# Performance work log

Measured on AMD Instinct MI355X. Metric: run time of the kernel, lower is better.

Reference implementation:

```python
import jax, jax.numpy as jnp
import numpy as np

B, S, HID = 2, 2048, 2048
NH, DN, DR, DV, RANK = 16, 128, 64, 128, 512
DQK = DN + DR
SCALE = DQK ** -0.5
EPS = 1e-5


def _rope(x, theta):
    # x: [..., d] with d even; theta broadcastable to [..., d//2] (angle per pair)
    x1, x2 = x[..., 0::2], x[..., 1::2]
    c, s = jnp.cos(theta), jnp.sin(theta)
    return jnp.stack([x1 * c - x2 * s, x1 * s + x2 * c], axis=-1).reshape(x.shape)


def _layernorm(x, gamma, beta):
    mu = jnp.mean(x, axis=-1, keepdims=True)
    var = jnp.var(x, axis=-1, keepdims=True)
    return (x - mu) * jax.lax.rsqrt(var + EPS) * gamma + beta


def setup_inputs() -> dict:
    key = jax.random.key(0)
    ks = jax.random.split(key, 8)
    def xavier(k, fan_in, fan_out, gain=1.0):
        lim = gain * np.sqrt(6.0 / (fan_in + fan_out))
        return jax.random.uniform(k, (fan_in, fan_out), jnp.float32, -lim, lim)
    return {
        "hidden_states": jax.random.normal(ks[0], (B, S, HID), jnp.float32),
        "freqs_cis": jax.random.uniform(ks[1], (S, DR // 2), jnp.float32) * 2.0 * np.pi,
        "Wq": xavier(ks[2], HID, NH * DQK),                      # q_proj (stored [in,out])
        "Wkv_a": xavier(ks[3], HID, RANK + DR),                  # kv_proj_a
        "kv_gamma": jnp.ones((RANK,), jnp.float32),              # kv_norm
        "kv_beta": jnp.zeros((RANK,), jnp.float32),
        "Wkv_b": xavier(ks[4], RANK, NH * (DN + DV)),            # kv_proj_b
        "Wout": xavier(ks[5], NH * DV, HID, gain=1.0 / np.sqrt(2.0)),  # out_proj
    }


def reference(hidden_states, freqs_cis, Wq, Wkv_a, kv_gamma, kv_beta, Wkv_b, Wout):
    b, s, _ = hidden_states.shape
    max_len = freqs_cis.shape[0]
    pos = jnp.arange(s) % max_len                      # [s], position_ids=None path
    theta = freqs_cis[pos]                             # [s, DR//2]

    # Q projection, split nope/rope, partial RoPE
    q = (hidden_states @ Wq).reshape(b, s, NH, DQK)
    q_nope, q_rope = q[..., :DN], q[..., DN:]
    q_rope = _rope(q_rope, theta[None, :, None, :])    # [b,s,nh,DR]

    # Low-rank KV: compressed latent + shared rope key
    kv = hidden_states @ Wkv_a                         # [b,s,RANK+DR]
    kv_c, k_rope = kv[..., :RANK], kv[..., RANK:]
    k_rope = _rope(k_rope, theta[None, :, :])          # [b,s,DR]
    kv_c = _layernorm(kv_c, kv_gamma, kv_beta)
    kvb = (kv_c @ Wkv_b).reshape(b, s, NH, DN + DV)
    k_nope, v = kvb[..., :DN], kvb[..., DN:]
    k = jnp.concatenate(
        [k_nope, jnp.broadcast_to(k_rope[:, :, None, :], (b, s, NH, DR))], axis=-1)

    q = jnp.concatenate([q_nope, q_rope], axis=-1)     # [b,s,nh,DQK]
    scores = jnp.einsum('bthd,bshd->btsh', q, k) * SCALE
    weights = jax.nn.softmax(scores.astype(jnp.float32), axis=2).astype(q.dtype)
    attn = jnp.einsum('btsh,bshd->bthd', weights, v).reshape(b, s, NH * DV)
    return attn @ Wout
```

## Files before the change

kernel.cpp:

```cpp
#include <hip/hip_runtime.h>

#define BATCH 2
#define SEQ   2048
#define HID   2048
#define NH    16
#define DN    128
#define DR    64
#define DV    128
#define RANK  512
#define DQK   192
#define NQ    (NH*DQK)
#define NQKV  3712
#define NKVB  (NH*(DN+DV))
#define NTOK  (BATCH*SEQ)
#define SCALE_F 0.07216878364870323f

typedef __bf16 bf16x8 __attribute__((ext_vector_type(8)));
typedef float  f32x4  __attribute__((ext_vector_type(4)));
typedef unsigned int u32x4 __attribute__((ext_vector_type(4)));
typedef unsigned short u16;
typedef unsigned short u16x4 __attribute__((ext_vector_type(4)));

__device__ __forceinline__ float b2f(u16 h) {
    unsigned int u = ((unsigned int)h) << 16;
    float f; __builtin_memcpy(&f, &u, 4); return f;
}
__device__ __forceinline__ u16 f2b(float f) {
    unsigned int x; __builtin_memcpy(&x, &f, 4);
    unsigned int r = x + 0x7fffu + ((x >> 16) & 1u);
    return (u16)(r >> 16);
}
__device__ __forceinline__ bf16x8 lds_frag(const u16* p) {
    u32x4 v = *(const u32x4*)p;
    return __builtin_bit_cast(bf16x8, v);
}
__device__ __forceinline__ bf16x8 to_frag(u32x4 v) {
    return __builtin_bit_cast(bf16x8, v);
}
__device__ __forceinline__ f32x4 mfma16(bf16x8 a, bf16x8 b, f32x4 c) {
    return __builtin_amdgcn_mfma_f32_16x16x32_bf16(a, b, c, 0, 0, 0);
}
__device__ __forceinline__ void store_out(u16* p, float v) { *p = f2b(v); }
__device__ __forceinline__ void store_out(float* p, float v) { *p = v; }
__device__ __forceinline__ void gld_lds16(const u16* g, u16* l) {
    __builtin_amdgcn_global_load_lds(
        (const __attribute__((address_space(1))) unsigned int*)g,
        (__attribute__((address_space(3))) unsigned int*)l, 16, 0, 0);
}

__global__ __launch_bounds__(256) void prep_kernel(
        const float* __restrict__ hs_f, u16* __restrict__ hs,
        const float* __restrict__ Wq, const float* __restrict__ Wkva,
        const float* __restrict__ Wkvb, const float* __restrict__ Wout,
        u16* __restrict__ WqkvT, u16* __restrict__ WkvbT, u16* __restrict__ WoutT) {
    int tid = threadIdx.x;
    int bid = blockIdx.x;
    if (bid < 8192) {
        int i = bid * 256 + tid;
        f32x4 v = *(const f32x4*)(hs_f + (size_t)i * 4);
        u16 o[4];
        for (int k = 0; k < 4; k++) o[k] = f2b(v[k]);
        *(unsigned long long*)(hs + (size_t)i * 4) = *(unsigned long long*)o;
        return;
    }
    bid -= 8192;
    const float* in; u16* out; int R, C, tilesC;
    if (bid < 1536)      { in = Wq;   out = WqkvT;                       R = HID;  C = NQ;   tilesC = 48; }
    else if (bid < 1856) { bid -= 1536; in = Wkva; out = WqkvT + (size_t)NQ * HID; R = HID; C = 576; tilesC = 10; }
    else if (bid < 2368) { bid -= 1856; in = Wkvb; out = WkvbT;          R = RANK; C = NKVB; tilesC = 64; }
    else                 { bid -= 2368; in = Wout; out = WoutT;          R = HID;  C = HID;  tilesC = 32; }
    __shared__ unsigned int t32[64 * 65];
    int r0 = (bid / tilesC) * 64, c0 = (bid % tilesC) * 64;
    bool valid = (c0 < C);
    for (int i = 0; i < 4; i++) {
        int u = tid + i * 256;
        int rl = u >> 4, c4 = u & 15;
        f32x4 v = {0.f, 0.f, 0.f, 0.f};
        if (valid) v = *(const f32x4*)&in[(size_t)(r0 + rl) * C + c0 + c4 * 4];
        for (int j = 0; j < 4; j++)
            t32[(c4 * 4 + j) * 65 + rl] = f2b(v[j]);
    }
    __syncthreads();
    for (int i = 0; i < 2; i++) {
        int u = tid + i * 256;
        int cl = u >> 3, r8 = (u & 7) * 8;
        unsigned int w[8];
        for (int j = 0; j < 8; j++) w[j] = t32[cl * 65 + r8 + j];
        u32x4 pk;
        for (int j = 0; j < 4; j++) pk[j] = (w[2 * j] & 0xffffu) | (w[2 * j + 1] << 16);
        *(u32x4*)&out[(size_t)(c0 + cl) * R + r0 + r8] = pk;
    }
}

template <typename OutT>
__global__ __launch_bounds__(256) void gemm_bt(const u16* __restrict__ A,
                                               const u16* __restrict__ Bt,
                                               OutT* __restrict__ C,
                                               int K, int lda, int ldb, int ldc) {
    __shared__ u16 As[128 * 32];
    __shared__ u16 Bs[128 * 32];
    int tid = threadIdx.x, lane = tid & 63, w = tid >> 6;
    int wm = (w >> 1) * 64, wn = (w & 1) * 64;
    int g = lane >> 4, ln = lane & 15;
    int m0 = blockIdx.y * 128, n0 = blockIdx.x * 128;
    f32x4 acc[4][4] = {};
    for (int k0 = 0; k0 < K; k0 += 32) {
        for (int i = 0; i < 2; i++) {
            int ch = tid + i * 256;
            int row = ch >> 2, o = ch & 3;
            gld_lds16(&A[(size_t)(m0 + row) * lda + k0 + o * 8], &As[row * 32 + o * 8]);
            gld_lds16(&Bt[(size_t)(n0 + row) * ldb + k0 + o * 8], &Bs[row * 32 + o * 8]);
        }
        __syncthreads();
        bf16x8 af[4], bf[4];
        for (int i = 0; i < 4; i++) af[i] = lds_frag(&As[(wm + i * 16 + ln) * 32 + g * 8]);
        for (int j = 0; j < 4; j++) bf[j] = lds_frag(&Bs[(wn + j * 16 + ln) * 32 + g * 8]);
        for (int i = 0; i < 4; i++)
            for (int j = 0; j < 4; j++)
                acc[i][j] = mfma16(af[i], bf[j], acc[i][j]);
        __syncthreads();
    }
    for (int i = 0; i < 4; i++)
        for (int j = 0; j < 4; j++)
            for (int r = 0; r < 4; r++) {
                int m = m0 + wm + i * 16 + g * 4 + r;
                int n = n0 + wn + j * 16 + ln;
                store_out(&C[(size_t)m * ldc + n], acc[i][j][r]);
            }
}

__global__ void rope_q(u16* __restrict__ qkv, const float* __restrict__ freqs) {
    int token = blockIdx.x;
    int s = token & (SEQ - 1);
    int tid = threadIdx.x;
    for (int i = 0; i < 2; i++) {
        int idx = tid + i * 256;
        int hh = idx >> 5, p = idx & 31;
        float th = freqs[s * 32 + p];
        float c = __cosf(th), sn = __sinf(th);
        size_t off = (size_t)token * NQKV + hh * DQK + DN + 2 * p;
        float x1 = b2f(qkv[off]), x2 = b2f(qkv[off + 1]);
        qkv[off]     = f2b(x1 * c - x2 * sn);
        qkv[off + 1] = f2b(x1 * sn + x2 * c);
    }
}

__global__ void ln_kv(const u16* __restrict__ qkv, const float* __restrict__ gamma,
                      const float* __restrict__ beta, u16* __restrict__ kv_c) {
    int row = blockIdx.x, tid = threadIdx.x;
    size_t base = (size_t)row * NQKV + NQ;
    float x0 = b2f(qkv[base + tid]), x1 = b2f(qkv[base + 256 + tid]);
    float s = x0 + x1, q2 = x0 * x0 + x1 * x1;
    for (int o = 32; o > 0; o >>= 1) { s += __shfl_xor(s, o); q2 += __shfl_xor(q2, o); }
    __shared__ float sh[8];
    int lane = tid & 63, w = tid >> 6;
    if (lane == 0) { sh[w] = s; sh[4 + w] = q2; }
    __syncthreads();
    float S = sh[0] + sh[1] + sh[2] + sh[3];
    float Q2 = sh[4] + sh[5] + sh[6] + sh[7];
    float mu = S * (1.f / 512.f);
    float var = Q2 * (1.f / 512.f) - mu * mu;
    float rs = rsqrtf(var + 1e-5f);
    kv_c[(size_t)row * RANK + tid] =
        f2b((x0 - mu) * rs * gamma[tid] + beta[tid]);
    kv_c[(size_t)row * RANK + 256 + tid] =
        f2b((x1 - mu) * rs * gamma[256 + tid] + beta[256 + tid]);
}

__global__ void k_assemble(const u16* __restrict__ kvb, const u16* __restrict__ qkv,
                           const float* __restrict__ freqs, u16* __restrict__ Kf) {
    int token = blockIdx.x;
    int s = token & (SEQ - 1);
    int tid = threadIdx.x;
    __shared__ u16 roped[64];
    if (tid < 32) {
        int p = tid;
        float th = freqs[s * 32 + p];
        float c = __cosf(th), sn = __sinf(th);
        float x1 = b2f(qkv[(size_t)token * NQKV + NQ + RANK + 2 * p]);
        float x2 = b2f(qkv[(size_t)token * NQKV + NQ + RANK + 2 * p + 1]);
        roped[2 * p]     = f2b(x1 * c - x2 * sn);
        roped[2 * p + 1] = f2b(x1 * sn + x2 * c);
    }
    __syncthreads();
    {
        int hh = tid >> 4, d8 = (tid & 15) * 8;
        *(u32x4*)&Kf[(size_t)token * NQ + hh * DQK + d8] =
            *(const u32x4*)&kvb[(size_t)token * NKVB + hh * 256 + d8];
    }
    if (tid < 128) {
        int hh = tid >> 3, d8 = (tid & 7) * 8;
        *(u32x4*)&Kf[(size_t)token * NQ + hh * DQK + DN + d8] = *(u32x4*)&roped[d8];
    }
}

__global__ void v_transpose(const u16* __restrict__ kvb, u16* __restrict__ Vt) {
    __shared__ unsigned int t32[64 * 65];
    int st = blockIdx.x * 64, dt = blockIdx.y * 64;
    int b = blockIdx.z >> 4, h = blockIdx.z & 15;
    int tid = threadIdx.x;
    for (int i = 0; i < 2; i++) {
        int u = tid + i * 256;
        int sl = u >> 3, c8 = (u & 7) * 8;
        u32x4 v = *(const u32x4*)&kvb[((size_t)(b * SEQ + st + sl) * NH + h) * 256 + DN + dt + c8];
        for (int j = 0; j < 4; j++) {
            t32[(c8 + 2 * j) * 65 + sl]     = v[j] & 0xffffu;
            t32[(c8 + 2 * j + 1) * 65 + sl] = v[j] >> 16;
        }
    }
    __syncthreads();
    for (int i = 0; i < 2; i++) {
        int u = tid + i * 256;
        int dl = u >> 3, s8 = (u & 7) * 8;
        unsigned int w[8];
        for (int j = 0; j < 8; j++) w[j] = t32[dl * 65 + s8 + j];
        u32x4 pk;
        for (int j = 0; j < 4; j++) pk[j] = (w[2 * j] & 0xffffu) | (w[2 * j + 1] << 16);
        *(u32x4*)&Vt[((size_t)(b * NH + h) * DV + dt + dl) * SEQ + st + s8] = pk;
    }
}

#define KC    64
#define QTILE 64
#define QSTR 200
#define PSTR 72
#define VSTR 72
#define NIT  (SEQ / KC)
__global__ __launch_bounds__(256, 3) void attn_kernel(const u16* __restrict__ Q,
                                                      const u16* __restrict__ Kf,
                                                      const u16* __restrict__ Vt,
                                                      u16* __restrict__ O) {
    __shared__ u16 Ks[KC * QSTR];
    __shared__ u16 Ps[QTILE * PSTR];
    __shared__ u16 Vs[DV * VSTR];
    __shared__ float lsumLDS[2][QTILE];
    int tid = threadIdx.x, lane = tid & 63, w = tid >> 6;
    int w1 = w & 1;
    int w2 = w >> 1;
    int g = lane >> 4, ln = lane & 15;
    int qt = blockIdx.x, h = blockIdx.y, b = blockIdx.z;

    size_t qbase  = ((size_t)(b * SEQ + qt * QTILE)) * NQKV + h * DQK;
    size_t kbase0 = ((size_t)(b * SEQ) * NH + h) * DQK;
    size_t vbase  = (size_t)(b * NH + h) * DV * SEQ;

    bf16x8 bfq[2][6];
    for (int ni = 0; ni < 2; ni++)
        for (int kk = 0; kk < 6; kk++)
            bfq[ni][kk] = to_frag(*(const u32x4*)&Q[qbase +
                (size_t)(w1 * 32 + ni * 16 + ln) * NQKV + kk * 32 + g * 8]);

    u32x4 kpre[6], vpre[4];
    {
        int krow = tid >> 2;
        for (int i = 0; i < 6; i++) {
            int o = (tid & 3) + 4 * i;
            kpre[i] = *(const u32x4*)&Kf[kbase0 + (size_t)krow * NQ + o * 8];
        }
        int vrow = tid >> 1;
        for (int i = 0; i < 4; i++) {
            int o = (tid & 1) + 2 * i;
            vpre[i] = *(const u32x4*)&Vt[vbase + (size_t)vrow * SEQ + o * 8];
        }
    }
    f32x4 oacc[2][4] = {};
    float lpriv[2] = {0.f, 0.f};

    for (int kt = 0; kt < NIT; kt++) {
        {
            int krow = tid >> 2;
            for (int i = 0; i < 6; i++) {
                int o = (tid & 3) + 4 * i;
                *(u32x4*)&Ks[krow * QSTR + o * 8] = kpre[i];
            }
            int vrow = tid >> 1;
            for (int i = 0; i < 4; i++) {
                int o = (tid & 1) + 2 * i;
                *(u32x4*)&Vs[vrow * VSTR + o * 8] = vpre[i];
            }
        }
        __syncthreads();
        if (kt + 1 < NIT) {
            size_t kb = kbase0 + (size_t)(kt + 1) * KC * NQ;
            int krow = tid >> 2;
            for (int i = 0; i < 6; i++) {
                int o = (tid & 3) + 4 * i;
                kpre[i] = *(const u32x4*)&Kf[kb + (size_t)krow * NQ + o * 8];
            }
            int vrow = tid >> 1;
            int c0 = (kt + 1) * KC;
            for (int i = 0; i < 4; i++) {
                int o = (tid & 1) + 2 * i;
                vpre[i] = *(const u32x4*)&Vt[vbase + (size_t)vrow * SEQ + c0 + o * 8];
            }
        }
        f32x4 sacc[2][2] = {};
        for (int kk = 0; kk < 6; kk++) {
            bf16x8 af[2];
            for (int mi = 0; mi < 2; mi++)
                af[mi] = lds_frag(&Ks[(w2 * 32 + mi * 16 + ln) * QSTR + kk * 32 + g * 8]);
            for (int mi = 0; mi < 2; mi++)
                for (int ni = 0; ni < 2; ni++)
                    sacc[mi][ni] = mfma16(af[mi], bfq[ni][kk], sacc[mi][ni]);
        }
        for (int mi = 0; mi < 2; mi++)
            for (int ni = 0; ni < 2; ni++) {
                float p0 = __expf(sacc[mi][ni][0] * SCALE_F);
                float p1 = __expf(sacc[mi][ni][1] * SCALE_F);
                float p2 = __expf(sacc[mi][ni][2] * SCALE_F);
                float p3 = __expf(sacc[mi][ni][3] * SCALE_F);
                lpriv[ni] += (p0 + p1) + (p2 + p3);
                u16x4 pk = { f2b(p0), f2b(p1), f2b(p2), f2b(p3) };
                *(u16x4*)&Ps[(w1 * 32 + ni * 16 + ln) * PSTR + (w2 * 32 + mi * 16 + g * 4)] = pk;
            }
        __syncthreads();
        for (int kk = 0; kk < 2; kk++) {
            bf16x8 pa[2], vb[4];
            for (int mi = 0; mi < 2; mi++)
                pa[mi] = lds_frag(&Ps[(w1 * 32 + mi * 16 + ln) * PSTR + kk * 32 + g * 8]);
            for (int ni = 0; ni < 4; ni++)
                vb[ni] = lds_frag(&Vs[(w2 * 64 + ni * 16 + ln) * VSTR + kk * 32 + g * 8]);
            for (int mi = 0; mi < 2; mi++)
                for (int ni = 0; ni < 4; ni++)
                    oacc[mi][ni] = mfma16(pa[mi], vb[ni], oacc[mi][ni]);
        }
        __syncthreads();
    }

    for (int ni = 0; ni < 2; ni++) {
        float v = lpriv[ni];
        v += __shfl_xor(v, 16);
        v += __shfl_xor(v, 32);
        if (g == 0) lsumLDS[w2][w1 * 32 + ni * 16 + ln] = v;
    }
    __syncthreads();
    for (int mi = 0; mi < 2; mi++)
        for (int ni = 0; ni < 4; ni++) {
            int d = w2 * 64 + ni * 16 + ln;
            for (int r = 0; r < 4; r++) {
                int row = w1 * 32 + mi * 16 + g * 4 + r;
                float l = lsumLDS[0][row] + lsumLDS[1][row];
                O[((size_t)(b * SEQ + qt * QTILE + row) * NH + h) * DV + d] =
                    f2b(oacc[mi][ni][r] / l);
            }
        }
}

extern "C" void kernel_launch(void* const* d_in, const int* in_sizes, int n_in,
                              void* d_out, int out_size, void* d_ws, size_t ws_size,
                              hipStream_t stream) {
    const float* hs_f  = (const float*)d_in[0];
    const float* freqs = (const float*)d_in[1];
    const float* Wq    = (const float*)d_in[2];
    const float* Wkva  = (const float*)d_in[3];
    const float* gamma = (const float*)d_in[4];
    const float* beta  = (const float*)d_in[5];
    const float* Wkvb  = (const float*)d_in[6];
    const float* Wout  = (const float*)d_in[7];
    float* outp = (float*)d_out;

    char* ws = (char*)d_ws;
    size_t off = 0;
    auto alloc = [&](size_t elems) -> u16* {
        u16* p = (u16*)(ws + off);
        off += ((elems * 2 + 255) / 256) * 256;
        return p;
    };
    u16* hs     = alloc((size_t)NTOK * HID);
    u16* WqkvT  = alloc((size_t)NQKV * HID);
    u16* WkvbT  = alloc((size_t)NKVB * RANK);
    u16* WoutT  = alloc((size_t)HID * HID);
    u16* qkv    = alloc((size_t)NTOK * NQKV);
    u16* kv_c   = alloc((size_t)NTOK * RANK);
    u16* kvb    = alloc((size_t)NTOK * NKVB);
    u16* Kf     = alloc((size_t)NTOK * NQ);
    u16* Vt     = alloc((size_t)BATCH * NH * DV * SEQ);
    u16* attn   = alloc((size_t)NTOK * NH * DV);
    (void)ws_size; (void)in_sizes; (void)n_in; (void)out_size;

    prep_kernel<<<8192 + 1536 + 320 + 512 + 1024, 256, 0, stream>>>(
        hs_f, hs, Wq, Wkva, Wkvb, Wout, WqkvT, WkvbT, WoutT);

    gemm_bt<<<dim3(NQKV / 128, NTOK / 128), 256, 0, stream>>>(hs, WqkvT, qkv, HID, HID, HID, NQKV);

    rope_q<<<NTOK, 256, 0, stream>>>(qkv, freqs);

    ln_kv<<<NTOK, 256, 0, stream>>>(qkv, gamma, beta, kv_c);

    gemm_bt<<<dim3(NKVB / 128, NTOK / 128), 256, 0, stream>>>(kv_c, WkvbT, kvb, RANK, RANK, RANK, NKVB);

    k_assemble<<<NTOK, 256, 0, stream>>>(kvb, qkv, freqs, Kf);

    v_transpose<<<dim3(SEQ / 64, DV / 64, BATCH * NH), 256, 0, stream>>>(kvb, Vt);

    attn_kernel<<<dim3(SEQ / QTILE, NH, BATCH), 256, 0, stream>>>(qkv, Kf, Vt, attn);

    gemm_bt<<<dim3(HID / 128, NTOK / 128), 256, 0, stream>>>(attn, WoutT, outp, HID, HID, HID, HID);
}
```

Before: 482.2 us.

## Swizzle K/V LDS tiles, use exp2 and packed bf16 conversion in attention

Replaces the padded row-major K and V shared-memory tiles with XOR-swizzled 64-byte-row slabs, one slab per 32-wide k chunk, so fragment reads and writes avoid bank conflicts without padding. The shared-memory footprint shrinks slightly. The softmax exponent becomes exp2f with the scale pre-multiplied by log2(e). The software float-to-bf16 rounding is replaced with the hardware v_cvt_pk_bf16_f32 packed conversion. The swizzle address math has to match the MFMA fragment layout exactly, or results will be wrong.

Result: no change. 479.2 us (-0.6%).

```diff
diff --git a/kernel.cpp b/kernel.cpp
--- a/kernel.cpp
+++ b/kernel.cpp
@@ -14,6 +14,7 @@
 #define NKVB  (NH*(DN+DV))
 #define NTOK  (BATCH*SEQ)
 #define SCALE_F 0.07216878364870323f
+#define SCALE_LOG2E 0.10411754831420211f
 
 typedef __bf16 bf16x8 __attribute__((ext_vector_type(8)));
 typedef float  f32x4  __attribute__((ext_vector_type(4)));
@@ -222,17 +223,15 @@
 
 #define KC    64
 #define QTILE 64
-#define QSTR 200
 #define PSTR 72
-#define VSTR 72
 #define NIT  (SEQ / KC)
 __global__ __launch_bounds__(256, 3) void attn_kernel(const u16* __restrict__ Q,
                                                       const u16* __restrict__ Kf,
                                                       const u16* __restrict__ Vt,
                                                       u16* __restrict__ O) {
-    __shared__ u16 Ks[KC * QSTR];
+    __shared__ u16 Ks[6 * 64 * 32];
+    __shared__ u16 Vs[2 * 128 * 32];
     __shared__ u16 Ps[QTILE * PSTR];
-    __shared__ u16 Vs[DV * VSTR];
     __shared__ float lsumLDS[2][QTILE];
     int tid = threadIdx.x, lane = tid & 63, w = tid >> 6;
     int w1 = w & 1;
@@ -250,14 +249,23 @@
             bfq[ni][kk] = to_frag(*(const u32x4*)&Q[qbase +
                 (size_t)(w1 * 32 + ni * 16 + ln) * NQKV + kk * 32 + g * 8]);
 
+    int rswz = ((ln >> 1) & 3) << 4;
+    int gb16 = g * 16;
+    int kRd[2], vRd[4];
+    for (int mi = 0; mi < 2; mi++) kRd[mi] = (w2 * 32 + mi * 16 + ln) * 64 + (gb16 ^ rswz);
+    for (int ni = 0; ni < 4; ni++) vRd[ni] = (w2 * 64 + ni * 16 + ln) * 64 + (gb16 ^ rswz);
+    int krow = tid >> 2, vrow = tid >> 1;
+    int kswz = ((krow >> 1) & 3) << 4, vswz = ((vrow >> 1) & 3) << 4;
+    int kWr  = krow * 64 + (((tid & 3) * 16) ^ kswz);
+    int vWr0 = vrow * 64 + (((tid & 1) * 16) ^ vswz);
+    int vWr1 = vrow * 64 + ((((tid & 1) + 2) * 16) ^ vswz);
+
     u32x4 kpre[6], vpre[4];
     {
-        int krow = tid >> 2;
         for (int i = 0; i < 6; i++) {
             int o = (tid & 3) + 4 * i;
             kpre[i] = *(const u32x4*)&Kf[kbase0 + (size_t)krow * NQ + o * 8];
         }
-        int vrow = tid >> 1;
         for (int i = 0; i < 4; i++) {
             int o = (tid & 1) + 2 * i;
             vpre[i] = *(const u32x4*)&Vt[vbase + (size_t)vrow * SEQ + o * 8];
@@ -267,27 +275,17 @@
     float lpriv[2] = {0.f, 0.f};
 
     for (int kt = 0; kt < NIT; kt++) {
-        {
-            int krow = tid >> 2;
-            for (int i = 0; i < 6; i++) {
-                int o = (tid & 3) + 4 * i;
-                *(u32x4*)&Ks[krow * QSTR + o * 8] = kpre[i];
-            }
-            int vrow = tid >> 1;
-            for (int i = 0; i < 4; i++) {
-                int o = (tid & 1) + 2 * i;
-                *(u32x4*)&Vs[vrow * VSTR + o * 8] = vpre[i];
-            }
-        }
+        for (int i = 0; i < 6; i++)
+            *(u32x4*)((char*)Ks + i * 4096 + kWr) = kpre[i];
+        for (int i = 0; i < 4; i++)
+            *(u32x4*)((char*)Vs + (i >> 1) * 8192 + ((i & 1) ? vWr1 : vWr0)) = vpre[i];
         __syncthreads();
         if (kt + 1 < NIT) {
             size_t kb = kbase0 + (size_t)(kt + 1) * KC * NQ;
-            int krow = tid >> 2;
             for (int i = 0; i < 6; i++) {
                 int o = (tid & 3) + 4 * i;
                 kpre[i] = *(const u32x4*)&Kf[kb + (size_t)krow * NQ + o * 8];
             }
-            int vrow = tid >> 1;
             int c0 = (kt + 1) * KC;
             for (int i = 0; i < 4; i++) {
                 int o = (tid & 1) + 2 * i;
@@ -298,20 +296,23 @@
         for (int kk = 0; kk < 6; kk++) {
             bf16x8 af[2];
             for (int mi = 0; mi < 2; mi++)
-                af[mi] = lds_frag(&Ks[(w2 * 32 + mi * 16 + ln) * QSTR + kk * 32 + g * 8]);
+                af[mi] = lds_frag((const u16*)((const char*)Ks + kk * 4096 + kRd[mi]));
             for (int mi = 0; mi < 2; mi++)
                 for (int ni = 0; ni < 2; ni++)
                     sacc[mi][ni] = mfma16(af[mi], bfq[ni][kk], sacc[mi][ni]);
         }
         for (int mi = 0; mi < 2; mi++)
             for (int ni = 0; ni < 2; ni++) {
-                float p0 = __expf(sacc[mi][ni][0] * SCALE_F);
-                float p1 = __expf(sacc[mi][ni][1] * SCALE_F);
-                float p2 = __expf(sacc[mi][ni][2] * SCALE_F);
-                float p3 = __expf(sacc[mi][ni][3] * SCALE_F);
+                float p0 = exp2f(sacc[mi][ni][0] * SCALE_LOG2E);
+                float p1 = exp2f(sacc[mi][ni][1] * SCALE_LOG2E);
+                float p2 = exp2f(sacc[mi][ni][2] * SCALE_LOG2E);
+                float p3 = exp2f(sacc[mi][ni][3] * SCALE_LOG2E);
                 lpriv[ni] += (p0 + p1) + (p2 + p3);
-                u16x4 pk = { f2b(p0), f2b(p1), f2b(p2), f2b(p3) };
-                *(u16x4*)&Ps[(w1 * 32 + ni * 16 + ln) * PSTR + (w2 * 32 + mi * 16 + g * 4)] = pk;
+                unsigned int q0, q1;
+                asm("v_cvt_pk_bf16_f32 %0, %1, %2" : "=v"(q0) : "v"(p0), "v"(p1));
+                asm("v_cvt_pk_bf16_f32 %0, %1, %2" : "=v"(q1) : "v"(p2), "v"(p3));
+                uint2 pk; pk.x = q0; pk.y = q1;
+                *(uint2*)&Ps[(w1 * 32 + ni * 16 + ln) * PSTR + (w2 * 32 + mi * 16 + g * 4)] = pk;
             }
         __syncthreads();
         for (int kk = 0; kk < 2; kk++) {
@@ -319,7 +320,7 @@
             for (int mi = 0; mi < 2; mi++)
                 pa[mi] = lds_frag(&Ps[(w1 * 32 + mi * 16 + ln) * PSTR + kk * 32 + g * 8]);
             for (int ni = 0; ni < 4; ni++)
-                vb[ni] = lds_frag(&Vs[(w2 * 64 + ni * 16 + ln) * VSTR + kk * 32 + g * 8]);
+                vb[ni] = lds_frag((const u16*)((const char*)Vs + kk * 8192 + vRd[ni]));
             for (int mi = 0; mi < 2; mi++)
                 for (int ni = 0; ni < 4; ni++)
                     oacc[mi][ni] = mfma16(pa[mi], vb[ni], oacc[mi][ni]);
```
